# Performance work log

Hardware: AMD Instinct MI355X
Metric: run time of the kernel (lower is better)

The kernel has to match this reference:

```python
import jax, jax.numpy as jnp
import numpy as np

INF = 1e10
D_KEY = 64

def setup_inputs() -> dict:
    key = jax.random.key(0)
    k1, k2, k3 = jax.random.split(key, 3)
    B, S, D = 4, 4096, D_KEY
    return {
        "query": jax.random.normal(k1, (B, S, D), dtype=jnp.float32),
        "key": jax.random.normal(k2, (B, S, D), dtype=jnp.float32),
        "value": jax.random.normal(k3, (B, S, D), dtype=jnp.float32),
        "mask": jnp.ones((B, S), dtype=jnp.float32),
    }

def reference(query, key, value, mask):
    # dot_products: [B, Sq, Sk]
    dot = jnp.einsum('bqd,bkd->bqk', query, key)
    S = key.shape[1]
    # causal: subtract INF on strict upper triangle (triu(1))
    tri = jnp.triu(jnp.ones((S, S), dtype=dot.dtype), 1) * INF
    dot = dot - tri[None, :, :]
    # additive padding mask: subtract (1-mask)*INF broadcast over query dim
    dot = dot - (1.0 - mask)[:, None, :] * INF
    scale = jnp.sqrt(jnp.float32(D_KEY))
    probs = jax.nn.softmax(dot / scale, axis=-1)  # [B, Sq, Sk]
    # dropout ratio = 0.0 -> identity
    return jnp.einsum('bqk,bkd->bqd', probs, value)
```

## Files before the change

kernel.cpp:

```cpp
#include <hip/hip_runtime.h>
#include <hip/hip_bf16.h>


#define S_LEN  4096
#define N_B    4
#define NT64   64
#define BIGF   1.803368e9f
#define QSCALE (0.125f * 1.44269504089f)
#define FIXMAX 11.0f
#define BIGNEG 1.25e9f
#define MADD_PAD 4224

typedef __attribute__((ext_vector_type(8))) short short8;
typedef __attribute__((ext_vector_type(4))) float f32x4;
typedef __attribute__((ext_vector_type(2))) unsigned int uint2v;
typedef __attribute__((ext_vector_type(4))) unsigned int uint4v;
typedef unsigned short ushort_t;

#define KT2_OFF   0
#define KT2_BYTES (N_B * NT64 * 4096 * 2)
#define VT2_OFF   (KT2_OFF + KT2_BYTES)
#define VT2_BYTES (N_B * NT64 * 4096 * 2)
#define NSLOT     (N_B * 184 * 4)
#define OP_OFF    (VT2_OFF + VT2_BYTES)
#define OP_BYTES  (NSLOT * 1024 * 4)
#define PLS_OFF   (OP_OFF + OP_BYTES)
#define PLS_BYTES (NSLOT * 32 * 4)
#define MADD_OFF  (PLS_OFF + PLS_BYTES)
#define MADD_BYTES (N_B * MADD_PAD * 4)
#define FLAG_OFF  (MADD_OFF + MADD_BYTES)
#define WS6_NEEDED (FLAG_OFF + 64)

__device__ __forceinline__ unsigned short f2bf(float f) {
    union { float f; unsigned u; } v; v.f = f;
    unsigned r = v.u + 0x7FFF + ((v.u >> 16) & 1);
    return (unsigned short)(r >> 16);
}
__device__ __forceinline__ float bflo(unsigned u) {
    union { unsigned u; float f; } v; v.u = u << 16; return v.f;
}
__device__ __forceinline__ float bfhi(unsigned u) {
    union { unsigned u; float f; } v; v.u = u & 0xffff0000u; return v.f;
}
__device__ __forceinline__ void ld_lds16(const void* g, void* l) {
    __builtin_amdgcn_global_load_lds((const __attribute__((address_space(1))) void*)g,
                                     (__attribute__((address_space(3))) void*)l, 16, 0, 0);
}


__global__ __launch_bounds__(256)
void prep5(const float* __restrict__ K, const float* __restrict__ V,
           const float* __restrict__ M,
           ushort_t* __restrict__ Kt, ushort_t* __restrict__ Vt,
           float* __restrict__ Madd, unsigned* __restrict__ Flag)
{
    const int t = blockIdx.x, b = blockIdx.y, tid = threadIdx.x;
    ushort_t* ko = Kt + ((size_t)(b * NT64 + t)) * 4096;
    ushort_t* vo = Vt + ((size_t)(b * NT64 + t)) * 4096;
    #pragma unroll
    for (int i = 0; i < 2; ++i) {
        const int idx = tid + 256 * i;
        const int row = idx >> 3, cc = idx & 7;
        const float* src = K + ((size_t)(b * S_LEN + t * 64 + row)) * 64 + cc * 8;
        const f32x4 a = *(const f32x4*)src;
        const f32x4 d4 = *(const f32x4*)(src + 4);
        short8 w;
        w[0]=(short)f2bf(a[0]); w[1]=(short)f2bf(a[1]); w[2]=(short)f2bf(a[2]); w[3]=(short)f2bf(a[3]);
        w[4]=(short)f2bf(d4[0]); w[5]=(short)f2bf(d4[1]); w[6]=(short)f2bf(d4[2]); w[7]=(short)f2bf(d4[3]);
        *(short8*)(ko + row * 64 + ((cc ^ (row & 7)) << 3)) = w;
    }
    #pragma unroll
    for (int i = 0; i < 2; ++i) {
        const int idx = tid + 256 * i;
        const int cc = idx >> 6, d = idx & 63;
        short8 w;
        #pragma unroll
        for (int j = 0; j < 8; ++j)
            w[j] = (short)f2bf(V[((size_t)(b * S_LEN + t * 64 + cc * 8 + j)) * 64 + d]);
        *(short8*)(vo + d * 64 + ((cc ^ (d & 7)) << 3)) = w;
    }
    if (tid < 64) {
        const int k = t * 64 + tid;
        const float mv = M[b * S_LEN + k];
        Madd[b * MADD_PAD + k] = (1.0f - mv) * BIGF;
        const unsigned long long nz = __ballot(mv != 1.0f);
        if (tid == 0 && nz) atomicOr(Flag, 1u);
    }
}

#define PTRANS(PA, PB, PF) do {                                                     \
    unsigned c00_, c01_, c10_, c11_;                                                \
    __asm__("v_cvt_pk_bf16_f32 %0, %1, %2" : "=v"(c00_) : "v"(PA[0]), "v"(PA[1])); \
    __asm__("v_cvt_pk_bf16_f32 %0, %1, %2" : "=v"(c01_) : "v"(PA[2]), "v"(PA[3])); \
    __asm__("v_cvt_pk_bf16_f32 %0, %1, %2" : "=v"(c10_) : "v"(PB[0]), "v"(PB[1])); \
    __asm__("v_cvt_pk_bf16_f32 %0, %1, %2" : "=v"(c11_) : "v"(PB[2]), "v"(PB[3])); \
    uint2v s0_ = __builtin_amdgcn_permlane32_swap(c00_, c10_, false, false);        \
    uint2v s1_ = __builtin_amdgcn_permlane32_swap(c01_, c11_, false, false);        \
    const unsigned T0_ = (unsigned)__builtin_amdgcn_ds_swizzle((int)s0_.x, 0x401F); \
    const unsigned T1_ = (unsigned)__builtin_amdgcn_ds_swizzle((int)s1_.x, 0x401F); \
    const unsigned U0_ = (unsigned)__builtin_amdgcn_ds_swizzle((int)s0_.y, 0x401F); \
    const unsigned U1_ = (unsigned)__builtin_amdgcn_ds_swizzle((int)s1_.y, 0x401F); \
    union { unsigned u[4]; short8 s; } pw_;                                         \
    pw_.u[0] = evn ? s0_.x : U0_;                                                   \
    pw_.u[1] = evn ? s1_.x : U1_;                                                   \
    pw_.u[2] = evn ? T0_ : s0_.y;                                                   \
    pw_.u[3] = evn ? T1_ : s1_.y;                                                   \
    PF = pw_.s;                                                                     \
} while (0)

#define CMASK(SV, BB, QG) do {                     \
    _Pragma("unroll")                              \
    for (int r_ = 0; r_ < 4; ++r_)                 \
        if ((BB) + r_ > (QG)) SV[r_] -= BIGF;      \
} while (0)

__global__ __launch_bounds__(256, 3)
void attn_fa9(const float* __restrict__ Q, const ushort_t* __restrict__ Kt,
              const ushort_t* __restrict__ Vt, const float* __restrict__ Madd,
              const unsigned* __restrict__ Flag,
              unsigned* __restrict__ Opu, float* __restrict__ Pll,
              float* __restrict__ O)
{
    const int x = 186 - blockIdx.x;
    const int b = blockIdx.y;
    int v = 1;
    #pragma unroll
    for (int vv = 2; vv <= 11; ++vv) v += (x >= (3 * vv * (vv - 1)) / 2) ? 1 : 0;
    const int y  = x - (3 * v * (v - 1)) / 2;
    const int T  = 3 * (v - 1) + y / v;
    const int c  = y - (y / v) * v;
    const int nt = 2 * T + 2;
    const int t0 = 6 * c;
    const int t1 = (t0 + 6 < nt) ? t0 + 6 : nt;

    const unsigned anymask = *Flag;

    const int wid  = threadIdx.x >> 6;
    const int lane = threadIdx.x & 63, l15 = lane & 15, g = lane >> 4;
    const bool evn = ((lane & 16) == 0);
    const int qbase = T * 128 + wid * 32;
    const int dtile = 2 * T + (wid >> 1);
    const int qg0 = 32 * (wid & 1) + l15 - 4 * g;
    const int qg1 = qg0 + 16;

    __shared__ __attribute__((aligned(16))) ushort_t Kb[2][4096];
    __shared__ __attribute__((aligned(16))) ushort_t Vb[2][4096];

    const float* Q0 = Q + ((size_t)(b * S_LEN + qbase + l15)) * 64 + g * 8;
    short8 qA0, qA1, qB0, qB1;
    {
        const f32x4 a0 = *(const f32x4*)(Q0);
        const f32x4 a1 = *(const f32x4*)(Q0 + 4);
        const f32x4 a2 = *(const f32x4*)(Q0 + 32);
        const f32x4 a3 = *(const f32x4*)(Q0 + 36);
        const float* Q1 = Q0 + 16 * 64;
        const f32x4 b0 = *(const f32x4*)(Q1);
        const f32x4 b1 = *(const f32x4*)(Q1 + 4);
        const f32x4 b2 = *(const f32x4*)(Q1 + 32);
        const f32x4 b3 = *(const f32x4*)(Q1 + 36);
        #pragma unroll
        for (int j = 0; j < 4; ++j) {
            qA0[j]     = (short)f2bf(a0[j] * QSCALE);
            qA0[4 + j] = (short)f2bf(a1[j] * QSCALE);
            qA1[j]     = (short)f2bf(a2[j] * QSCALE);
            qA1[4 + j] = (short)f2bf(a3[j] * QSCALE);
            qB0[j]     = (short)f2bf(b0[j] * QSCALE);
            qB0[4 + j] = (short)f2bf(b1[j] * QSCALE);
            qB1[j]     = (short)f2bf(b2[j] * QSCALE);
            qB1[4 + j] = (short)f2bf(b3[j] * QSCALE);
        }
    }
    short8 ones8;
    #pragma unroll
    for (int j = 0; j < 8; ++j) ones8[j] = (short)0x3F80;

    const char*  KtB = (const char*)Kt + (size_t)b * (NT64 * 8192);
    const char*  VtB = (const char*)Vt + (size_t)b * (NT64 * 8192);
    const float* MaB = Madd + (size_t)b * MADD_PAD + 4 * g;

    f32x4 accA[5], accB[5];
    #pragma unroll
    for (int dt = 0; dt < 5; ++dt) {
        accA[dt] = (f32x4){0.f, 0.f, 0.f, 0.f};
        accB[dt] = (f32x4){0.f, 0.f, 0.f, 0.f};
    }

    auto stage = [&](int bf, int t_) {
        const char* kg = KtB + (size_t)t_ * 8192 + wid * 2048 + lane * 16;
        char* kl = (char*)&Kb[bf][0] + wid * 2048;
        ld_lds16(kg,        kl);
        ld_lds16(kg + 1024, kl + 1024);
        const char* vg = VtB + (size_t)t_ * 8192 + wid * 2048 + lane * 16;
        char* vl = (char*)&Vb[bf][0] + wid * 2048;
        ld_lds16(vg,        vl);
        ld_lds16(vg + 1024, vl + 1024);
    };

    stage(0, t0);
    int buf = 0;
    const int ch0 = ((g ^ (l15 & 7)) << 3);
    const int ch1 = (((4 | g) ^ (l15 & 7)) << 3);

    for (int t = t0; t < t1; ++t) {
        const bool live = (t <= dtile);
        f32x4 mm0, mm1, mm2, mm3;
        if (anymask && live) {
            const float* mp = MaB + t * 64;
            mm0 = *(const f32x4*)(mp);
            mm1 = *(const f32x4*)(mp + 16);
            mm2 = *(const f32x4*)(mp + 32);
            mm3 = *(const f32x4*)(mp + 48);
        }
        if (t + 1 < t1) {
            stage(buf ^ 1, t + 1);
            __asm__ volatile("s_waitcnt vmcnt(4)" ::: "memory");
        } else {
            __asm__ volatile("s_waitcnt vmcnt(0)" ::: "memory");
        }
        __builtin_amdgcn_s_barrier();
        __builtin_amdgcn_sched_barrier(0);

        if (live) {
            const ushort_t* kb = &Kb[buf][0];
            const f32x4 z_ = (f32x4){0.f, 0.f, 0.f, 0.f};
            short8 k00 = *(const short8*)(kb + ((0  + l15) << 6) + ch0);
            short8 k01 = *(const short8*)(kb + ((0  + l15) << 6) + ch1);
            short8 k10 = *(const short8*)(kb + ((16 + l15) << 6) + ch0);
            short8 k11 = *(const short8*)(kb + ((16 + l15) << 6) + ch1);
            short8 k20 = *(const short8*)(kb + ((32 + l15) << 6) + ch0);
            short8 k21 = *(const short8*)(kb + ((32 + l15) << 6) + ch1);
            short8 k30 = *(const short8*)(kb + ((48 + l15) << 6) + ch0);
            short8 k31 = *(const short8*)(kb + ((48 + l15) << 6) + ch1);

            f32x4 sA0 = __builtin_amdgcn_mfma_f32_16x16x32_bf16(k00, qA0, z_, 0, 0, 0);
            f32x4 sA1 = __builtin_amdgcn_mfma_f32_16x16x32_bf16(k10, qA0, z_, 0, 0, 0);
            f32x4 sA2 = __builtin_amdgcn_mfma_f32_16x16x32_bf16(k20, qA0, z_, 0, 0, 0);
            f32x4 sA3 = __builtin_amdgcn_mfma_f32_16x16x32_bf16(k30, qA0, z_, 0, 0, 0);
            f32x4 sB0 = __builtin_amdgcn_mfma_f32_16x16x32_bf16(k00, qB0, z_, 0, 0, 0);
            f32x4 sB1 = __builtin_amdgcn_mfma_f32_16x16x32_bf16(k10, qB0, z_, 0, 0, 0);
            f32x4 sB2 = __builtin_amdgcn_mfma_f32_16x16x32_bf16(k20, qB0, z_, 0, 0, 0);
            f32x4 sB3 = __builtin_amdgcn_mfma_f32_16x16x32_bf16(k30, qB0, z_, 0, 0, 0);
            sA0 = __builtin_amdgcn_mfma_f32_16x16x32_bf16(k01, qA1, sA0, 0, 0, 0);
            sA1 = __builtin_amdgcn_mfma_f32_16x16x32_bf16(k11, qA1, sA1, 0, 0, 0);
            sA2 = __builtin_amdgcn_mfma_f32_16x16x32_bf16(k21, qA1, sA2, 0, 0, 0);
            sA3 = __builtin_amdgcn_mfma_f32_16x16x32_bf16(k31, qA1, sA3, 0, 0, 0);
            sB0 = __builtin_amdgcn_mfma_f32_16x16x32_bf16(k01, qB1, sB0, 0, 0, 0);
            sB1 = __builtin_amdgcn_mfma_f32_16x16x32_bf16(k11, qB1, sB1, 0, 0, 0);
            sB2 = __builtin_amdgcn_mfma_f32_16x16x32_bf16(k21, qB1, sB2, 0, 0, 0);
            sB3 = __builtin_amdgcn_mfma_f32_16x16x32_bf16(k31, qB1, sB3, 0, 0, 0);

            if (anymask) {
                sA0 -= mm0; sA1 -= mm1; sA2 -= mm2; sA3 -= mm3;
                sB0 -= mm0; sB1 -= mm1; sB2 -= mm2; sB3 -= mm3;
            }
            if (t == dtile) {
                CMASK(sA0, 0, qg0); CMASK(sA1, 16, qg0);
                CMASK(sA2, 32, qg0); CMASK(sA3, 48, qg0);
                CMASK(sB0, 0, qg1); CMASK(sB1, 16, qg1);
                CMASK(sB2, 32, qg1); CMASK(sB3, 48, qg1);
            }

            float pa0[4], pa1[4], pa2[4], pa3[4];
            float pb0[4], pb1[4], pb2[4], pb3[4];
            #pragma unroll
            for (int r = 0; r < 4; ++r) {
                pa0[r] = exp2f(sA0[r] - FIXMAX);
                pa1[r] = exp2f(sA1[r] - FIXMAX);
                pa2[r] = exp2f(sA2[r] - FIXMAX);
                pa3[r] = exp2f(sA3[r] - FIXMAX);
                pb0[r] = exp2f(sB0[r] - FIXMAX);
                pb1[r] = exp2f(sB1[r] - FIXMAX);
                pb2[r] = exp2f(sB2[r] - FIXMAX);
                pb3[r] = exp2f(sB3[r] - FIXMAX);
            }

            short8 pAlo, pAhi, pBlo, pBhi;
            PTRANS(pa0, pa1, pAlo);
            PTRANS(pa2, pa3, pAhi);
            PTRANS(pb0, pb1, pBlo);
            PTRANS(pb2, pb3, pBhi);

            const ushort_t* vb = &Vb[buf][0];
            short8 vL0 = *(const short8*)(vb + ((0  + l15) << 6) + ch0);
            short8 vH0 = *(const short8*)(vb + ((0  + l15) << 6) + ch1);
            short8 vL1 = *(const short8*)(vb + ((16 + l15) << 6) + ch0);
            short8 vH1 = *(const short8*)(vb + ((16 + l15) << 6) + ch1);
            short8 vL2 = *(const short8*)(vb + ((32 + l15) << 6) + ch0);
            short8 vH2 = *(const short8*)(vb + ((32 + l15) << 6) + ch1);
            short8 vL3 = *(const short8*)(vb + ((48 + l15) << 6) + ch0);
            short8 vH3 = *(const short8*)(vb + ((48 + l15) << 6) + ch1);
            __builtin_amdgcn_s_setprio(1);
            accA[0] = __builtin_amdgcn_mfma_f32_16x16x32_bf16(pAlo, vL0, accA[0], 0, 0, 0);
            accA[1] = __builtin_amdgcn_mfma_f32_16x16x32_bf16(pAlo, vL1, accA[1], 0, 0, 0);
            accA[2] = __builtin_amdgcn_mfma_f32_16x16x32_bf16(pAlo, vL2, accA[2], 0, 0, 0);
            accA[3] = __builtin_amdgcn_mfma_f32_16x16x32_bf16(pAlo, vL3, accA[3], 0, 0, 0);
            accA[4] = __builtin_amdgcn_mfma_f32_16x16x32_bf16(pAlo, ones8, accA[4], 0, 0, 0);
            accB[0] = __builtin_amdgcn_mfma_f32_16x16x32_bf16(pBlo, vL0, accB[0], 0, 0, 0);
            accB[1] = __builtin_amdgcn_mfma_f32_16x16x32_bf16(pBlo, vL1, accB[1], 0, 0, 0);
            accB[2] = __builtin_amdgcn_mfma_f32_16x16x32_bf16(pBlo, vL2, accB[2], 0, 0, 0);
            accB[3] = __builtin_amdgcn_mfma_f32_16x16x32_bf16(pBlo, vL3, accB[3], 0, 0, 0);
            accB[4] = __builtin_amdgcn_mfma_f32_16x16x32_bf16(pBlo, ones8, accB[4], 0, 0, 0);
            accA[0] = __builtin_amdgcn_mfma_f32_16x16x32_bf16(pAhi, vH0, accA[0], 0, 0, 0);
            accA[1] = __builtin_amdgcn_mfma_f32_16x16x32_bf16(pAhi, vH1, accA[1], 0, 0, 0);
            accA[2] = __builtin_amdgcn_mfma_f32_16x16x32_bf16(pAhi, vH2, accA[2], 0, 0, 0);
            accA[3] = __builtin_amdgcn_mfma_f32_16x16x32_bf16(pAhi, vH3, accA[3], 0, 0, 0);
            accA[4] = __builtin_amdgcn_mfma_f32_16x16x32_bf16(pAhi, ones8, accA[4], 0, 0, 0);
            accB[0] = __builtin_amdgcn_mfma_f32_16x16x32_bf16(pBhi, vH0, accB[0], 0, 0, 0);
            accB[1] = __builtin_amdgcn_mfma_f32_16x16x32_bf16(pBhi, vH1, accB[1], 0, 0, 0);
            accB[2] = __builtin_amdgcn_mfma_f32_16x16x32_bf16(pBhi, vH2, accB[2], 0, 0, 0);
            accB[3] = __builtin_amdgcn_mfma_f32_16x16x32_bf16(pBhi, vH3, accB[3], 0, 0, 0);
            accB[4] = __builtin_amdgcn_mfma_f32_16x16x32_bf16(pBhi, ones8, accB[4], 0, 0, 0);
            __builtin_amdgcn_s_setprio(0);
        }

        __builtin_amdgcn_sched_barrier(0);
        __builtin_amdgcn_s_barrier();
        buf ^= 1;
    }

    if (v == 1) {
        float* Ob = O + ((size_t)(b * S_LEN + qbase)) * 64;
        #pragma unroll
        for (int r = 0; r < 4; ++r) {
            const float ila = 1.0f / accA[4][r];
            const float ilb = 1.0f / accB[4][r];
            #pragma unroll
            for (int dt = 0; dt < 4; ++dt) {
                Ob[(4 * g + r) * 64 + 16 * dt + l15]        = accA[dt][r] * ila;
                Ob[(16 + 4 * g + r) * 64 + 16 * dt + l15]   = accB[dt][r] * ilb;
            }
        }
    } else {
        const int slot = (b * 184 + (x - 3)) * 4 + wid;
        unsigned* Os = Opu + (size_t)slot * 1024;
        #pragma unroll
        for (int dt = 0; dt < 4; ++dt) {
            unsigned u0, u1, u2, u3;
            __asm__("v_cvt_pk_bf16_f32 %0, %1, %2" : "=v"(u0) : "v"(accA[dt][0]), "v"(accA[dt][1]));
            __asm__("v_cvt_pk_bf16_f32 %0, %1, %2" : "=v"(u1) : "v"(accA[dt][2]), "v"(accA[dt][3]));
            __asm__("v_cvt_pk_bf16_f32 %0, %1, %2" : "=v"(u2) : "v"(accB[dt][0]), "v"(accB[dt][1]));
            __asm__("v_cvt_pk_bf16_f32 %0, %1, %2" : "=v"(u3) : "v"(accB[dt][2]), "v"(accB[dt][3]));
            const int d = 16 * dt + l15;
            Os[(2 * g + 0) * 64 + d] = u0;
            Os[(2 * g + 1) * 64 + d] = u1;
            Os[(8 + 2 * g + 0) * 64 + d] = u2;
            Os[(8 + 2 * g + 1) * 64 + d] = u3;
        }
        if (l15 == 0) {
            #pragma unroll
            for (int r = 0; r < 4; ++r) {
                Pll[slot * 32 + 4 * g + r]      = accA[4][r];
                Pll[slot * 32 + 16 + 4 * g + r] = accB[4][r];
            }
        }
    }
}

__global__ __launch_bounds__(256)
void combine6(const unsigned* __restrict__ Opu, const float* __restrict__ Pll,
              float* __restrict__ O)
{
    const int bx = blockIdx.x, b = blockIdx.y;
    const int T = 3 + (bx >> 2), wv = bx & 3;
    const int v = (T + 3) / 3;
    const int x0 = (3 * v * (v - 1)) / 2 + (T - 3 * (v - 1)) * v;
    const int sb = (b * 184 + (x0 - 3)) * 4 + wv;
    const int tid = threadIdx.x, rg = tid >> 6, d = tid & 63;

    float a[8] = {0.f,0.f,0.f,0.f,0.f,0.f,0.f,0.f};
    float l[8] = {0.f,0.f,0.f,0.f,0.f,0.f,0.f,0.f};
    for (int cc = 0; cc < v; ++cc) {
        const int sl = sb + 4 * cc;
        const uint4v pu = *(const uint4v*)&Opu[(size_t)sl * 1024 + (4 * rg) * 64 + d];
        const unsigned* base = &Opu[(size_t)sl * 1024 + d];
        const unsigned w0 = base[(4 * rg + 0) * 64];
        const unsigned w1 = base[(4 * rg + 1) * 64];
        const unsigned w2 = base[(4 * rg + 2) * 64];
        const unsigned w3 = base[(4 * rg + 3) * 64];
        (void)pu;
        a[0] += bflo(w0); a[1] += bfhi(w0);
        a[2] += bflo(w1); a[3] += bfhi(w1);
        a[4] += bflo(w2); a[5] += bfhi(w2);
        a[6] += bflo(w3); a[7] += bfhi(w3);
        #pragma unroll
        for (int j = 0; j < 8; ++j)
            l[j] += Pll[sl * 32 + 8 * rg + j];
    }
    float* Ob = O + ((size_t)(b * S_LEN + T * 128 + wv * 32 + 8 * rg)) * 64 + d;
    #pragma unroll
    for (int j = 0; j < 8; ++j)
        Ob[(size_t)j * 64] = a[j] / l[j];
}


__global__ __launch_bounds__(256)
void attn_fwd_fb(const float* __restrict__ Q, const float* __restrict__ K,
                 const float* __restrict__ V, const float* __restrict__ M,
                 float* __restrict__ O)
{
    const int tile  = blockIdx.x;
    const int b     = blockIdx.y;
    const int qbase = tile * 64;
    const int tid   = threadIdx.x;
    const int wave  = tid >> 6;
    const int lane  = tid & 63;
    const int l15   = lane & 15;
    const int g     = lane >> 4;

    __shared__ __attribute__((aligned(16))) unsigned short Klds[32 * 64];
    __shared__ __attribute__((aligned(16))) unsigned short Vtlds[64 * 40];
    __shared__ __attribute__((aligned(16))) unsigned short Plds[4][16 * 40];

    const float* Qb = Q + ((size_t)b * S_LEN + qbase) * 64;
    const float* Kb = K + (size_t)b * S_LEN * 64;
    const float* Vb = V + (size_t)b * S_LEN * 64;
    const float* Mb = M + (size_t)b * S_LEN;

    const int qrow = 16 * wave + l15;
    short8 qf[2];
    #pragma unroll
    for (int dc = 0; dc < 2; ++dc) {
        const float* src = Qb + (size_t)qrow * 64 + dc * 32 + g * 8;
        #pragma unroll
        for (int j = 0; j < 8; ++j) qf[dc][j] = (short)f2bf(src[j] * 0.125f);
    }

    f32x4 acc[4];
    #pragma unroll
    for (int dt = 0; dt < 4; ++dt) acc[dt] = (f32x4){0.f, 0.f, 0.f, 0.f};
    float mrow[4], lrow[4];
    #pragma unroll
    for (int r = 0; r < 4; ++r) { mrow[r] = -1e30f; lrow[r] = 0.f; }

    const int q_max_wave = qbase + 16 * wave + 15;
    const int nkv = (qbase + 64) / 32;

    for (int it = 0; it < nkv; ++it) {
        const int kv = it * 32;
        __syncthreads();
        {
            const int k = tid >> 3, c = tid & 7;
            const float* src = Kb + (size_t)(kv + k) * 64 + c * 8;
            short8 t8;
            #pragma unroll
            for (int j = 0; j < 8; ++j) t8[j] = (short)f2bf(src[j]);
            const int byte = k * 128 + ((c * 16) ^ ((k & 7) << 4));
            *(short8*)((char*)Klds + byte) = t8;
        }
        {
            const int k = tid & 31, dch = tid >> 5;
            const float* src = Vb + (size_t)(kv + k) * 64 + dch * 8;
            #pragma unroll
            for (int j = 0; j < 8; ++j)
                Vtlds[(dch * 8 + j) * 40 + k] = f2bf(src[j]);
        }
        __syncthreads();

        if (kv > q_max_wave) continue;

        f32x4 s[2];
        s[0] = (f32x4){0.f,0.f,0.f,0.f};
        s[1] = (f32x4){0.f,0.f,0.f,0.f};
        #pragma unroll
        for (int kt = 0; kt < 2; ++kt) {
            const int krow = 16 * kt + l15;
            #pragma unroll
            for (int dc = 0; dc < 2; ++dc) {
                const int byte = krow * 128 + ((dc * 64 + g * 16) ^ ((krow & 7) << 4));
                short8 kf = *(const short8*)((const char*)Klds + byte);
                s[kt] = __builtin_amdgcn_mfma_f32_16x16x32_bf16(qf[dc], kf, s[kt], 0, 0, 0);
            }
        }

        float mk0 = Mb[kv + l15];
        float mk1 = Mb[kv + 16 + l15];
        #pragma unroll
        for (int kt = 0; kt < 2; ++kt) {
            const int gk = kv + 16 * kt + l15;
            const float madd = (1.0f - (kt ? mk1 : mk0)) * BIGNEG;
            #pragma unroll
            for (int r = 0; r < 4; ++r) {
                const int gq = qbase + 16 * wave + 4 * g + r;
                float vv = s[kt][r] - madd;
                if (gk > gq) vv -= BIGNEG;
                s[kt][r] = vv;
            }
        }

        float pexp[2][4], alpha[4];
        #pragma unroll
        for (int r = 0; r < 4; ++r) {
            float tm = fmaxf(s[0][r], s[1][r]);
            #pragma unroll
            for (int off = 8; off >= 1; off >>= 1)
                tm = fmaxf(tm, __shfl_xor(tm, off, 64));
            const float mnew = fmaxf(mrow[r], tm);
            const float a  = __expf(mrow[r] - mnew);
            const float p0 = __expf(s[0][r] - mnew);
            const float p1 = __expf(s[1][r] - mnew);
            float rs = p0 + p1;
            #pragma unroll
            for (int off = 8; off >= 1; off >>= 1)
                rs += __shfl_xor(rs, off, 64);
            lrow[r] = lrow[r] * a + rs;
            mrow[r] = mnew;
            alpha[r] = a;
            pexp[0][r] = p0; pexp[1][r] = p1;
        }

        #pragma unroll
        for (int dt = 0; dt < 4; ++dt)
            #pragma unroll
            for (int r = 0; r < 4; ++r)
                acc[dt][r] *= alpha[r];

        unsigned short* P = Plds[wave];
        #pragma unroll
        for (int kt = 0; kt < 2; ++kt)
            #pragma unroll
            for (int r = 0; r < 4; ++r)
                P[(4 * g + r) * 40 + 16 * kt + l15] = f2bf(pexp[kt][r]);

        __asm__ volatile("s_waitcnt lgkmcnt(0)" ::: "memory");

        short8 pf = *(const short8*)((const char*)P + (l15 * 40 + g * 8) * 2);
        #pragma unroll
        for (int dt = 0; dt < 4; ++dt) {
            short8 vf = *(const short8*)((const char*)Vtlds + ((dt * 16 + l15) * 40 + g * 8) * 2);
            acc[dt] = __builtin_amdgcn_mfma_f32_16x16x32_bf16(pf, vf, acc[dt], 0, 0, 0);
        }
    }

    float* Ob = O + ((size_t)b * S_LEN + qbase) * 64;
    #pragma unroll
    for (int r = 0; r < 4; ++r) {
        const float inv = 1.0f / lrow[r];
        const int row = 16 * wave + 4 * g + r;
        #pragma unroll
        for (int dt = 0; dt < 4; ++dt)
            Ob[(size_t)row * 64 + dt * 16 + l15] = acc[dt][r] * inv;
    }
}

extern "C" void kernel_launch(void* const* d_in, const int* in_sizes, int n_in,
                              void* d_out, int out_size, void* d_ws, size_t ws_size,
                              hipStream_t stream) {
    const float* Q = (const float*)d_in[0];
    const float* K = (const float*)d_in[1];
    const float* V = (const float*)d_in[2];
    const float* M = (const float*)d_in[3];
    float* O = (float*)d_out;

    if (ws_size >= (size_t)WS6_NEEDED) {
        ushort_t* Kt = (ushort_t*)((char*)d_ws + KT2_OFF);
        ushort_t* Vt = (ushort_t*)((char*)d_ws + VT2_OFF);
        unsigned* Op = (unsigned*)((char*)d_ws + OP_OFF);
        float*    Pll= (float*)((char*)d_ws + PLS_OFF);
        float*    Ma = (float*)((char*)d_ws + MADD_OFF);
        unsigned* Fl = (unsigned*)((char*)d_ws + FLAG_OFF);
        hipMemsetAsync(Fl, 0, 4, stream);
        prep5<<<dim3(NT64, N_B), 256, 0, stream>>>(K, V, M, Kt, Vt, Ma, Fl);
        attn_fa9<<<dim3(187, N_B), 256, 0, stream>>>(Q, Kt, Vt, Ma, Fl, Op, Pll, O);
        combine6<<<dim3(116, N_B), 256, 0, stream>>>(Op, Pll, O);
    } else {
        dim3 grid(S_LEN / 64, N_B);
        attn_fwd_fb<<<grid, 256, 0, stream>>>(Q, K, V, M, O);
    }
}
```

Before: 44.39 us.

## Triple-buffer K/V staging with one barrier per tile and LDS mask staging

Replaces the double-buffered K/V LDS pipeline, which needed two barriers per tile, with a three-slot ring. Loads run two tiles ahead and each iteration has a single barrier. The additive padding mask is now staged into LDS alongside K/V through global_load_lds and always applied. This drops the global any-mask flag, its memset and its atomic. The inner loop is also split into two 32-key halves to cut live registers, at the cost of more LDS use, which may lower occupancy under launch_bounds(256,3).

```diff
diff --git a/kernel.cpp b/kernel.cpp
--- a/kernel.cpp
+++ b/kernel.cpp
@@ -14,7 +14,6 @@
 typedef __attribute__((ext_vector_type(8))) short short8;
 typedef __attribute__((ext_vector_type(4))) float f32x4;
 typedef __attribute__((ext_vector_type(2))) unsigned int uint2v;
-typedef __attribute__((ext_vector_type(4))) unsigned int uint4v;
 typedef unsigned short ushort_t;
 
 #define KT2_OFF   0
@@ -28,8 +27,7 @@
 #define PLS_BYTES (NSLOT * 32 * 4)
 #define MADD_OFF  (PLS_OFF + PLS_BYTES)
 #define MADD_BYTES (N_B * MADD_PAD * 4)
-#define FLAG_OFF  (MADD_OFF + MADD_BYTES)
-#define WS6_NEEDED (FLAG_OFF + 64)
+#define WS7_NEEDED (MADD_OFF + MADD_BYTES)
 
 __device__ __forceinline__ unsigned short f2bf(float f) {
     union { float f; unsigned u; } v; v.f = f;
@@ -46,13 +44,17 @@
     __builtin_amdgcn_global_load_lds((const __attribute__((address_space(1))) void*)g,
                                      (__attribute__((address_space(3))) void*)l, 16, 0, 0);
 }
+__device__ __forceinline__ void ld_lds4(const void* g, void* l) {
+    __builtin_amdgcn_global_load_lds((const __attribute__((address_space(1))) void*)g,
+                                     (__attribute__((address_space(3))) void*)l, 4, 0, 0);
+}
 
 
 __global__ __launch_bounds__(256)
-void prep5(const float* __restrict__ K, const float* __restrict__ V,
+void prep6(const float* __restrict__ K, const float* __restrict__ V,
            const float* __restrict__ M,
            ushort_t* __restrict__ Kt, ushort_t* __restrict__ Vt,
-           float* __restrict__ Madd, unsigned* __restrict__ Flag)
+           float* __restrict__ Madd)
 {
     const int t = blockIdx.x, b = blockIdx.y, tid = threadIdx.x;
     ushort_t* ko = Kt + ((size_t)(b * NT64 + t)) * 4096;
@@ -81,10 +83,7 @@
     }
     if (tid < 64) {
         const int k = t * 64 + tid;
-        const float mv = M[b * S_LEN + k];
-        Madd[b * MADD_PAD + k] = (1.0f - mv) * BIGF;
-        const unsigned long long nz = __ballot(mv != 1.0f);
-        if (tid == 0 && nz) atomicOr(Flag, 1u);
+        Madd[b * MADD_PAD + k] = (1.0f - M[b * S_LEN + k]) * BIGF;
     }
 }
 
@@ -115,11 +114,10 @@
 } while (0)
 
 __global__ __launch_bounds__(256, 3)
-void attn_fa9(const float* __restrict__ Q, const ushort_t* __restrict__ Kt,
-              const ushort_t* __restrict__ Vt, const float* __restrict__ Madd,
-              const unsigned* __restrict__ Flag,
-              unsigned* __restrict__ Opu, float* __restrict__ Pll,
-              float* __restrict__ O)
+void attn_fa10(const float* __restrict__ Q, const ushort_t* __restrict__ Kt,
+               const ushort_t* __restrict__ Vt, const float* __restrict__ Madd,
+               unsigned* __restrict__ Opu, float* __restrict__ Pll,
+               float* __restrict__ O)
 {
     const int x = 186 - blockIdx.x;
     const int b = blockIdx.y;
@@ -133,8 +131,6 @@
     const int t0 = 6 * c;
     const int t1 = (t0 + 6 < nt) ? t0 + 6 : nt;
 
-    const unsigned anymask = *Flag;
-
     const int wid  = threadIdx.x >> 6;
     const int lane = threadIdx.x & 63, l15 = lane & 15, g = lane >> 4;
     const bool evn = ((lane & 16) == 0);
@@ -143,8 +139,9 @@
     const int qg0 = 32 * (wid & 1) + l15 - 4 * g;
     const int qg1 = qg0 + 16;
 
-    __shared__ __attribute__((aligned(16))) ushort_t Kb[2][4096];
-    __shared__ __attribute__((aligned(16))) ushort_t Vb[2][4096];
+    __shared__ __attribute__((aligned(16))) ushort_t Kb[3][4096];
+    __shared__ __attribute__((aligned(16))) ushort_t Vb[3][4096];
+    __shared__ __attribute__((aligned(16))) float    Ml[3][4][64];
 
     const float* Q0 = Q + ((size_t)(b * S_LEN + qbase + l15)) * 64 + g * 8;
     short8 qA0, qA1, qB0, qB1;
@@ -174,9 +171,9 @@
     #pragma unroll
     for (int j = 0; j < 8; ++j) ones8[j] = (short)0x3F80;
 
-    const char*  KtB = (const char*)Kt + (size_t)b * (NT64 * 8192);
-    const char*  VtB = (const char*)Vt + (size_t)b * (NT64 * 8192);
-    const float* MaB = Madd + (size_t)b * MADD_PAD + 4 * g;
+    const char*  KtB  = (const char*)Kt + (size_t)b * (NT64 * 8192);
+    const char*  VtB  = (const char*)Vt + (size_t)b * (NT64 * 8192);
+    const float* MaBs = Madd + (size_t)b * MADD_PAD;
 
     f32x4 accA[5], accB[5];
     #pragma unroll
@@ -185,137 +182,102 @@
         accB[dt] = (f32x4){0.f, 0.f, 0.f, 0.f};
     }
 
-    auto stage = [&](int bf, int t_) {
+    auto stage = [&](int sl, int t_) {
         const char* kg = KtB + (size_t)t_ * 8192 + wid * 2048 + lane * 16;
-        char* kl = (char*)&Kb[bf][0] + wid * 2048;
+        char* kl = (char*)&Kb[sl][0] + wid * 2048;
         ld_lds16(kg,        kl);
         ld_lds16(kg + 1024, kl + 1024);
         const char* vg = VtB + (size_t)t_ * 8192 + wid * 2048 + lane * 16;
-        char* vl = (char*)&Vb[bf][0] + wid * 2048;
+        char* vl = (char*)&Vb[sl][0] + wid * 2048;
         ld_lds16(vg,        vl);
         ld_lds16(vg + 1024, vl + 1024);
+        ld_lds4 (MaBs + (size_t)t_ * 64 + lane, &Ml[sl][wid][0]);
     };
 
     stage(0, t0);
-    int buf = 0;
+    if (t0 + 1 < t1) stage(1, t0 + 1);
+
     const int ch0 = ((g ^ (l15 & 7)) << 3);
     const int ch1 = (((4 | g) ^ (l15 & 7)) << 3);
 
+    int sc = 0;
     for (int t = t0; t < t1; ++t) {
-        const bool live = (t <= dtile);
-        f32x4 mm0, mm1, mm2, mm3;
-        if (anymask && live) {
-            const float* mp = MaB + t * 64;
-            mm0 = *(const f32x4*)(mp);
-            mm1 = *(const f32x4*)(mp + 16);
-            mm2 = *(const f32x4*)(mp + 32);
-            mm3 = *(const f32x4*)(mp + 48);
-        }
         if (t + 1 < t1) {
-            stage(buf ^ 1, t + 1);
-            __asm__ volatile("s_waitcnt vmcnt(4)" ::: "memory");
+            __asm__ volatile("s_waitcnt vmcnt(5)" ::: "memory");
         } else {
             __asm__ volatile("s_waitcnt vmcnt(0)" ::: "memory");
         }
         __builtin_amdgcn_s_barrier();
         __builtin_amdgcn_sched_barrier(0);
 
-        if (live) {
-            const ushort_t* kb = &Kb[buf][0];
+        const int sn = (sc + 2 > 2) ? sc - 1 : sc + 2;
+        if (t + 2 < t1) stage(sn, t + 2);
+
+        if (t <= dtile) {
+            const ushort_t* kbase = &Kb[sc][0];
+            const ushort_t* vbase = &Vb[sc][0];
+            const float*    mlw   = &Ml[sc][wid][0];
             const f32x4 z_ = (f32x4){0.f, 0.f, 0.f, 0.f};
-            short8 k00 = *(const short8*)(kb + ((0  + l15) << 6) + ch0);
-            short8 k01 = *(const short8*)(kb + ((0  + l15) << 6) + ch1);
-            short8 k10 = *(const short8*)(kb + ((16 + l15) << 6) + ch0);
-            short8 k11 = *(const short8*)(kb + ((16 + l15) << 6) + ch1);
-            short8 k20 = *(const short8*)(kb + ((32 + l15) << 6) + ch0);
-            short8 k21 = *(const short8*)(kb + ((32 + l15) << 6) + ch1);
-            short8 k30 = *(const short8*)(kb + ((48 + l15) << 6) + ch0);
-            short8 k31 = *(const short8*)(kb + ((48 + l15) << 6) + ch1);
-
-            f32x4 sA0 = __builtin_amdgcn_mfma_f32_16x16x32_bf16(k00, qA0, z_, 0, 0, 0);
-            f32x4 sA1 = __builtin_amdgcn_mfma_f32_16x16x32_bf16(k10, qA0, z_, 0, 0, 0);
-            f32x4 sA2 = __builtin_amdgcn_mfma_f32_16x16x32_bf16(k20, qA0, z_, 0, 0, 0);
-            f32x4 sA3 = __builtin_amdgcn_mfma_f32_16x16x32_bf16(k30, qA0, z_, 0, 0, 0);
-            f32x4 sB0 = __builtin_amdgcn_mfma_f32_16x16x32_bf16(k00, qB0, z_, 0, 0, 0);
-            f32x4 sB1 = __builtin_amdgcn_mfma_f32_16x16x32_bf16(k10, qB0, z_, 0, 0, 0);
-            f32x4 sB2 = __builtin_amdgcn_mfma_f32_16x16x32_bf16(k20, qB0, z_, 0, 0, 0);
-            f32x4 sB3 = __builtin_amdgcn_mfma_f32_16x16x32_bf16(k30, qB0, z_, 0, 0, 0);
-            sA0 = __builtin_amdgcn_mfma_f32_16x16x32_bf16(k01, qA1, sA0, 0, 0, 0);
-            sA1 = __builtin_amdgcn_mfma_f32_16x16x32_bf16(k11, qA1, sA1, 0, 0, 0);
-            sA2 = __builtin_amdgcn_mfma_f32_16x16x32_bf16(k21, qA1, sA2, 0, 0, 0);
-            sA3 = __builtin_amdgcn_mfma_f32_16x16x32_bf16(k31, qA1, sA3, 0, 0, 0);
-            sB0 = __builtin_amdgcn_mfma_f32_16x16x32_bf16(k01, qB1, sB0, 0, 0, 0);
-            sB1 = __builtin_amdgcn_mfma_f32_16x16x32_bf16(k11, qB1, sB1, 0, 0, 0);
-            sB2 = __builtin_amdgcn_mfma_f32_16x16x32_bf16(k21, qB1, sB2, 0, 0, 0);
-            sB3 = __builtin_amdgcn_mfma_f32_16x16x32_bf16(k31, qB1, sB3, 0, 0, 0);
-
-            if (anymask) {
-                sA0 -= mm0; sA1 -= mm1; sA2 -= mm2; sA3 -= mm3;
-                sB0 -= mm0; sB1 -= mm1; sB2 -= mm2; sB3 -= mm3;
+
+            #pragma unroll
+            for (int h = 0; h < 2; ++h) {
+                const int rb = 32 * h;
+                const int chh = h ? ch1 : ch0;
+                const f32x4 mmE = *(const f32x4*)(mlw + rb + 4 * g);
+                const f32x4 mmO = *(const f32x4*)(mlw + rb + 16 + 4 * g);
+
+                short8 ke0 = *(const short8*)(kbase + ((rb + l15) << 6) + ch0);
+                short8 ke1 = *(const short8*)(kbase + ((rb + l15) << 6) + ch1);
+                short8 ko0 = *(const short8*)(kbase + ((rb + 16 + l15) << 6) + ch0);
+                short8 ko1 = *(const short8*)(kbase + ((rb + 16 + l15) << 6) + ch1);
+
+                f32x4 sEA = __builtin_amdgcn_mfma_f32_16x16x32_bf16(ke0, qA0, z_, 0, 0, 0);
+                f32x4 sOA = __builtin_amdgcn_mfma_f32_16x16x32_bf16(ko0, qA0, z_, 0, 0, 0);
+                f32x4 sEB = __builtin_amdgcn_mfma_f32_16x16x32_bf16(ke0, qB0, z_, 0, 0, 0);
+                f32x4 sOB = __builtin_amdgcn_mfma_f32_16x16x32_bf16(ko0, qB0, z_, 0, 0, 0);
+                sEA = __builtin_amdgcn_mfma_f32_16x16x32_bf16(ke1, qA1, sEA, 0, 0, 0);
+                sOA = __builtin_amdgcn_mfma_f32_16x16x32_bf16(ko1, qA1, sOA, 0, 0, 0);
+                sEB = __builtin_amdgcn_mfma_f32_16x16x32_bf16(ke1, qB1, sEB, 0, 0, 0);
+                sOB = __builtin_amdgcn_mfma_f32_16x16x32_bf16(ko1, qB1, sOB, 0, 0, 0);
+
+                sEA -= mmE; sOA -= mmO; sEB -= mmE; sOB -= mmO;
+                if (t == dtile) {
+                    CMASK(sEA, rb, qg0);      CMASK(sOA, rb + 16, qg0);
+                    CMASK(sEB, rb, qg1);      CMASK(sOB, rb + 16, qg1);
+                }
+
+                float pEA[4], pOA[4], pEB[4], pOB[4];
+                #pragma unroll
+                for (int r = 0; r < 4; ++r) {
+                    pEA[r] = exp2f(sEA[r] - FIXMAX);
+                    pOA[r] = exp2f(sOA[r] - FIXMAX);
+                    pEB[r] = exp2f(sEB[r] - FIXMAX);
+                    pOB[r] = exp2f(sOB[r] - FIXMAX);
+                }
+
+                short8 pfA, pfB;
+                PTRANS(pEA, pOA, pfA);
+                PTRANS(pEB, pOB, pfB);
+
+                short8 v0 = *(const short8*)(vbase + ((0  + l15) << 6) + chh);
+                short8 v1 = *(const short8*)(vbase + ((16 + l15) << 6) + chh);
+                short8 v2 = *(const short8*)(vbase + ((32 + l15) << 6) + chh);
+                short8 v3 = *(const short8*)(vbase + ((48 + l15) << 6) + chh);
+                __builtin_amdgcn_s_setprio(1);
+                accA[0] = __builtin_amdgcn_mfma_f32_16x16x32_bf16(pfA, v0, accA[0], 0, 0, 0);
+                accA[1] = __builtin_amdgcn_mfma_f32_16x16x32_bf16(pfA, v1, accA[1], 0, 0, 0);
+                accA[2] = __builtin_amdgcn_mfma_f32_16x16x32_bf16(pfA, v2, accA[2], 0, 0, 0);
+                accA[3] = __builtin_amdgcn_mfma_f32_16x16x32_bf16(pfA, v3, accA[3], 0, 0, 0);
+                accA[4] = __builtin_amdgcn_mfma_f32_16x16x32_bf16(pfA, ones8, accA[4], 0, 0, 0);
+                accB[0] = __builtin_amdgcn_mfma_f32_16x16x32_bf16(pfB, v0, accB[0], 0, 0, 0);
+                accB[1] = __builtin_amdgcn_mfma_f32_16x16x32_bf16(pfB, v1, accB[1], 0, 0, 0);
+                accB[2] = __builtin_amdgcn_mfma_f32_16x16x32_bf16(pfB, v2, accB[2], 0, 0, 0);
+                accB[3] = __builtin_amdgcn_mfma_f32_16x16x32_bf16(pfB, v3, accB[3], 0, 0, 0);
+                accB[4] = __builtin_amdgcn_mfma_f32_16x16x32_bf16(pfB, ones8, accB[4], 0, 0, 0);
+                __builtin_amdgcn_s_setprio(0);
             }
-            if (t == dtile) {
-                CMASK(sA0, 0, qg0); CMASK(sA1, 16, qg0);
-                CMASK(sA2, 32, qg0); CMASK(sA3, 48, qg0);
-                CMASK(sB0, 0, qg1); CMASK(sB1, 16, qg1);
-                CMASK(sB2, 32, qg1); CMASK(sB3, 48, qg1);
-            }
-
-            float pa0[4], pa1[4], pa2[4], pa3[4];
-            float pb0[4], pb1[4], pb2[4], pb3[4];
-            #pragma unroll
-            for (int r = 0; r < 4; ++r) {
-                pa0[r] = exp2f(sA0[r] - FIXMAX);
-                pa1[r] = exp2f(sA1[r] - FIXMAX);
-                pa2[r] = exp2f(sA2[r] - FIXMAX);
-                pa3[r] = exp2f(sA3[r] - FIXMAX);
-                pb0[r] = exp2f(sB0[r] - FIXMAX);
-                pb1[r] = exp2f(sB1[r] - FIXMAX);
-                pb2[r] = exp2f(sB2[r] - FIXMAX);
-                pb3[r] = exp2f(sB3[r] - FIXMAX);
-            }
-
-            short8 pAlo, pAhi, pBlo, pBhi;
-            PTRANS(pa0, pa1, pAlo);
-            PTRANS(pa2, pa3, pAhi);
-            PTRANS(pb0, pb1, pBlo);
-            PTRANS(pb2, pb3, pBhi);
-
-            const ushort_t* vb = &Vb[buf][0];
-            short8 vL0 = *(const short8*)(vb + ((0  + l15) << 6) + ch0);
-            short8 vH0 = *(const short8*)(vb + ((0  + l15) << 6) + ch1);
-            short8 vL1 = *(const short8*)(vb + ((16 + l15) << 6) + ch0);
-            short8 vH1 = *(const short8*)(vb + ((16 + l15) << 6) + ch1);
-            short8 vL2 = *(const short8*)(vb + ((32 + l15) << 6) + ch0);
-            short8 vH2 = *(const short8*)(vb + ((32 + l15) << 6) + ch1);
-            short8 vL3 = *(const short8*)(vb + ((48 + l15) << 6) + ch0);
-            short8 vH3 = *(const short8*)(vb + ((48 + l15) << 6) + ch1);
-            __builtin_amdgcn_s_setprio(1);
-            accA[0] = __builtin_amdgcn_mfma_f32_16x16x32_bf16(pAlo, vL0, accA[0], 0, 0, 0);
-            accA[1] = __builtin_amdgcn_mfma_f32_16x16x32_bf16(pAlo, vL1, accA[1], 0, 0, 0);
-            accA[2] = __builtin_amdgcn_mfma_f32_16x16x32_bf16(pAlo, vL2, accA[2], 0, 0, 0);
-            accA[3] = __builtin_amdgcn_mfma_f32_16x16x32_bf16(pAlo, vL3, accA[3], 0, 0, 0);
-            accA[4] = __builtin_amdgcn_mfma_f32_16x16x32_bf16(pAlo, ones8, accA[4], 0, 0, 0);
-            accB[0] = __builtin_amdgcn_mfma_f32_16x16x32_bf16(pBlo, vL0, accB[0], 0, 0, 0);
-            accB[1] = __builtin_amdgcn_mfma_f32_16x16x32_bf16(pBlo, vL1, accB[1], 0, 0, 0);
-            accB[2] = __builtin_amdgcn_mfma_f32_16x16x32_bf16(pBlo, vL2, accB[2], 0, 0, 0);
-            accB[3] = __builtin_amdgcn_mfma_f32_16x16x32_bf16(pBlo, vL3, accB[3], 0, 0, 0);
-            accB[4] = __builtin_amdgcn_mfma_f32_16x16x32_bf16(pBlo, ones8, accB[4], 0, 0, 0);
-            accA[0] = __builtin_amdgcn_mfma_f32_16x16x32_bf16(pAhi, vH0, accA[0], 0, 0, 0);
-            accA[1] = __builtin_amdgcn_mfma_f32_16x16x32_bf16(pAhi, vH1, accA[1], 0, 0, 0);
-            accA[2] = __builtin_amdgcn_mfma_f32_16x16x32_bf16(pAhi, vH2, accA[2], 0, 0, 0);
-            accA[3] = __builtin_amdgcn_mfma_f32_16x16x32_bf16(pAhi, vH3, accA[3], 0, 0, 0);
-            accA[4] = __builtin_amdgcn_mfma_f32_16x16x32_bf16(pAhi, ones8, accA[4], 0, 0, 0);
-            accB[0] = __builtin_amdgcn_mfma_f32_16x16x32_bf16(pBhi, vH0, accB[0], 0, 0, 0);
-            accB[1] = __builtin_amdgcn_mfma_f32_16x16x32_bf16(pBhi, vH1, accB[1], 0, 0, 0);
-            accB[2] = __builtin_amdgcn_mfma_f32_16x16x32_bf16(pBhi, vH2, accB[2], 0, 0, 0);
-            accB[3] = __builtin_amdgcn_mfma_f32_16x16x32_bf16(pBhi, vH3, accB[3], 0, 0, 0);
-            accB[4] = __builtin_amdgcn_mfma_f32_16x16x32_bf16(pBhi, ones8, accB[4], 0, 0, 0);
-            __builtin_amdgcn_s_setprio(0);
-        }
-
-        __builtin_amdgcn_sched_barrier(0);
-        __builtin_amdgcn_s_barrier();
-        buf ^= 1;
+        }
+        sc = (sc == 2) ? 0 : sc + 1;
     }
 
     if (v == 1) {
@@ -326,8 +288,8 @@
             const float ilb = 1.0f / accB[4][r];
             #pragma unroll
             for (int dt = 0; dt < 4; ++dt) {
-                Ob[(4 * g + r) * 64 + 16 * dt + l15]        = accA[dt][r] * ila;
-                Ob[(16 + 4 * g + r) * 64 + 16 * dt + l15]   = accB[dt][r] * ilb;
+                Ob[(4 * g + r) * 64 + 16 * dt + l15]      = accA[dt][r] * ila;
+                Ob[(16 + 4 * g + r) * 64 + 16 * dt + l15] = accB[dt][r] * ilb;
             }
         }
     } else {
@@ -341,8 +303,8 @@
             __asm__("v_cvt_pk_bf16_f32 %0, %1, %2" : "=v"(u2) : "v"(accB[dt][0]), "v"(accB[dt][1]));
             __asm__("v_cvt_pk_bf16_f32 %0, %1, %2" : "=v"(u3) : "v"(accB[dt][2]), "v"(accB[dt][3]));
             const int d = 16 * dt + l15;
-            Os[(2 * g + 0) * 64 + d] = u0;
-            Os[(2 * g + 1) * 64 + d] = u1;
+            Os[(2 * g + 0) * 64 + d]     = u0;
+            Os[(2 * g + 1) * 64 + d]     = u1;
             Os[(8 + 2 * g + 0) * 64 + d] = u2;
             Os[(8 + 2 * g + 1) * 64 + d] = u3;
         }
@@ -371,13 +333,11 @@
     float l[8] = {0.f,0.f,0.f,0.f,0.f,0.f,0.f,0.f};
     for (int cc = 0; cc < v; ++cc) {
         const int sl = sb + 4 * cc;
-        const uint4v pu = *(const uint4v*)&Opu[(size_t)sl * 1024 + (4 * rg) * 64 + d];
         const unsigned* base = &Opu[(size_t)sl * 1024 + d];
         const unsigned w0 = base[(4 * rg + 0) * 64];
         const unsigned w1 = base[(4 * rg + 1) * 64];
         const unsigned w2 = base[(4 * rg + 2) * 64];
         const unsigned w3 = base[(4 * rg + 3) * 64];
-        (void)pu;
         a[0] += bflo(w0); a[1] += bfhi(w0);
         a[2] += bflo(w1); a[3] += bfhi(w1);
         a[4] += bflo(w2); a[5] += bfhi(w2);
@@ -551,16 +511,14 @@
     const float* M = (const float*)d_in[3];
     float* O = (float*)d_out;
 
-    if (ws_size >= (size_t)WS6_NEEDED) {
+    if (ws_size >= (size_t)WS7_NEEDED) {
         ushort_t* Kt = (ushort_t*)((char*)d_ws + KT2_OFF);
         ushort_t* Vt = (ushort_t*)((char*)d_ws + VT2_OFF);
         unsigned* Op = (unsigned*)((char*)d_ws + OP_OFF);
         float*    Pll= (float*)((char*)d_ws + PLS_OFF);
         float*    Ma = (float*)((char*)d_ws + MADD_OFF);
-        unsigned* Fl = (unsigned*)((char*)d_ws + FLAG_OFF);
-        hipMemsetAsync(Fl, 0, 4, stream);
-        prep5<<<dim3(NT64, N_B), 256, 0, stream>>>(K, V, M, Kt, Vt, Ma, Fl);
-        attn_fa9<<<dim3(187, N_B), 256, 0, stream>>>(Q, Kt, Vt, Ma, Fl, Op, Pll, O);
+        prep6<<<dim3(NT64, N_B), 256, 0, stream>>>(K, V, M, Kt, Vt, Ma);
+        attn_fa10<<<dim3(187, N_B), 256, 0, stream>>>(Q, Kt, Vt, Ma, Op, Pll, O);
         combine6<<<dim3(116, N_B), 256, 0, stream>>>(Op, Pll, O);
     } else {
         dim3 grid(S_LEN / 64, N_B);
```

Result: faster. 40.64 us (-8.4%).
